# Optimization experiments

Hardware: AMD Instinct MI355X
Metric: run time of the kernel (lower is better)

## Reference

```python
import jax, jax.numpy as jnp
import numpy as np
from jax import lax

KERNEL = 2
STACKS = 2
LAYERS = 10
DILATIONS = [2 ** l for _ in range(STACKS) for l in range(LAYERS)]  # 20 blocks
RECEPTIVE_FIELD = sum((KERNEL - 1) * d for d in DILATIONS)  # 2046


def setup_inputs() -> dict:
    key = jax.random.key(0)
    ks = jax.random.split(key, 8)
    B, L, C, NC = 8, 4096, 256, 256
    NB = len(DILATIONS)
    SK = L - RECEPTIVE_FIELD  # 2050

    def rn(k, shape, scale):
        return jax.random.normal(k, shape, jnp.float32) * scale

    return {
        "input_x": jax.random.normal(ks[0], (B, L, 1), jnp.float32),
        "causal_w": rn(ks[1], (1, C), 1.0),                 # 1x1 causal conv, in=1
        "causal_b": jnp.zeros((C,), jnp.float32),
        "dil_w": rn(ks[2], (NB, KERNEL, C, C), (KERNEL * C) ** -0.5),  # WIO per block
        "dil_b": jnp.zeros((NB, C), jnp.float32),
        "res_w": rn(ks[3], (NB, C, C), C ** -0.5),
        "res_b": jnp.zeros((NB, C), jnp.float32),
        "skip_w": rn(ks[4], (NB, C, C), C ** -0.5),
        "skip_b": jnp.zeros((NB, C), jnp.float32),
        "cls_conv_w": rn(ks[5], (C, C), C ** -0.5),
        "cls_conv_b": jnp.zeros((C,), jnp.float32),
        "dense_w": rn(ks[6], (SK * C, NC), (SK * C) ** -0.5),
        "dense_b": jnp.zeros((NC,), jnp.float32),
    }


def _conv1x1(x, w, b):
    # x: [B, T, Cin], w: [Cin, Cout]
    return jnp.einsum("btc,co->bto", x, w) + b


def _dilated_causal_conv(x, w, b, d):
    # keras 'causal' pad followed by slicing off the first (k-1)*d frames
    # is exactly a VALID dilated conv. x: [B,T,Cin], w: [K,Cin,Cout]
    y = lax.conv_general_dilated(
        x, w, window_strides=(1,), padding="VALID", rhs_dilation=(d,),
        dimension_numbers=("NWC", "WIO", "NWC"))
    return y + b


def reference(input_x, causal_w, causal_b, dil_w, dil_b, res_w, res_b,
              skip_w, skip_b, cls_conv_w, cls_conv_b, dense_w, dense_b):
    # initial causal conv (kernel_size=1 -> plain 1x1 conv)
    x = _conv1x1(input_x, causal_w, causal_b)  # [B, L, C]
    skip_size = x.shape[1] - RECEPTIVE_FIELD

    skips = []
    for i, d in enumerate(DILATIONS):
        h = _dilated_causal_conv(x, dil_w[i], dil_b[i], d)  # [B, T-(k-1)d, C]
        g = jnp.tanh(h) * jax.nn.sigmoid(h)                  # gated activation
        res = _conv1x1(g, res_w[i], res_b[i])
        x = res + g                                          # residual (same length)
        s = _conv1x1(g, skip_w[i], skip_b[i])[:, -skip_size:]
        skips.append(s)

    # classifier head: mean over blocks, relu, shared 1x1 conv twice, dense+softmax
    s = jnp.mean(jnp.stack(skips, 0), axis=0)  # [B, skip_size, C]
    s = jax.nn.relu(s)
    s = _conv1x1(s, cls_conv_w, cls_conv_b)
    s = jax.nn.relu(s)
    s = _conv1x1(s, cls_conv_w, cls_conv_b)    # same conv applied twice (shared weights)
    f = s.reshape(s.shape[0], -1)              # flatten [B, skip_size*C]
    logits = f @ dense_w + dense_b
    return jax.nn.softmax(logits, axis=-1)
```

## Files before the change

### kernel.cpp

```cpp
#include <hip/hip_runtime.h>

typedef __attribute__((ext_vector_type(8))) short short8;
typedef __attribute__((ext_vector_type(4))) float f32x4;
typedef unsigned int uint32;
typedef unsigned short u16;

#define CCH   256
#define BATCH 8
#define LFULL 4096
#define SKL   2050
#define BM    128
#define BN    128
#define LDK   72

#define GSTRIDE ((size_t)BATCH * LFULL * CCH)
#define XSTR    ((size_t)LFULL * CCH)
#define SSTR    ((size_t)SKL * CCH)
#define PSTR    ((size_t)BATCH * SKL * CCH)

__device__ const int TOUT[20] = {4095,4093,4089,4081,4065,4033,3969,3841,3585,3073,
                                 3072,3070,3066,3058,3042,3010,2946,2818,2562,2050};

__device__ __forceinline__ u16 f2b(float f) {
  uint32 u = __float_as_uint(f);
  u += 0x7fff + ((u >> 16) & 1);
  return (u16)(u >> 16);
}
__device__ __forceinline__ float gatef(float h) {
  float hc = fmaxf(h, -30.0f);
  float q = __expf(-hc);
  return (1.0f - q) * __builtin_amdgcn_rcpf(fmaf(q, q, 1.0f));
}
__device__ __forceinline__ void glds16(const void* g, void* l) {
  __builtin_amdgcn_global_load_lds(
      (const __attribute__((address_space(1))) void*)g,
      (__attribute__((address_space(3))) void*)l, 16, 0, 0);
}

__global__ __launch_bounds__(256)
void compose_w(const float* __restrict__ res_w, const float* __restrict__ dil_w,
               u16* __restrict__ DWc) {
  __shared__ float As[32][256];
  int bx = blockIdx.x;
  int chunk = bx & 7, tap = (bx >> 3) & 1, bi = bx >> 4;
  int i = bi + 1;
  int co = threadIdx.x;
  int ci0 = chunk * 32;

  for (int idx = threadIdx.x; idx < 32 * 256; idx += 256) {
    int r = idx >> 8, m = idx & 255;
    float v = res_w[((size_t)(bi * 256 + ci0 + r)) * 256 + m];
    if (ci0 + r == m) v += 1.0f;
    As[r][m] = v;
  }
  __syncthreads();

  float acc[32];
  #pragma unroll
  for (int r = 0; r < 32; ++r) acc[r] = 0.0f;

  const float* Wb = dil_w + ((size_t)(i * 2 + tap) * 256) * 256 + co;
  for (int m4 = 0; m4 < 64; ++m4) {
    const float* wp = Wb + (size_t)m4 * 4 * 256;
    float w0 = wp[0], w1 = wp[256], w2 = wp[512], w3 = wp[768];
    #pragma unroll
    for (int r = 0; r < 32; ++r) {
      float4 a = *(const float4*)&As[r][m4 * 4];
      acc[r] = fmaf(a.x, w0, acc[r]);
      acc[r] = fmaf(a.y, w1, acc[r]);
      acc[r] = fmaf(a.z, w2, acc[r]);
      acc[r] = fmaf(a.w, w3, acc[r]);
    }
  }
  u16* op = DWc + ((size_t)(bi * 256 + co)) * 512 + tap * 256 + ci0;
  #pragma unroll
  for (int r = 0; r < 32; ++r) op[r] = f2b(acc[r]);
}

__global__ __launch_bounds__(256)
void compose_bias(const float* __restrict__ res_b, const float* __restrict__ dil_w,
                  const float* __restrict__ dil_b, float* __restrict__ Bc) {
  int bi = blockIdx.x, i = bi + 1, co = threadIdx.x;
  float acc = dil_b[(size_t)i * 256 + co];
  const float* W0 = dil_w + ((size_t)(i * 2 + 0) * 256) * 256;
  const float* W1 = dil_w + ((size_t)(i * 2 + 1) * 256) * 256;
  for (int m = 0; m < 256; ++m) {
    float rb = res_b[(size_t)bi * 256 + m];
    acc = fmaf(rb, W0[(size_t)m * 256 + co] + W1[(size_t)m * 256 + co], acc);
  }
  Bc[(size_t)bi * 256 + co] = acc;
}

__global__ __launch_bounds__(256)
void head0(const float* __restrict__ causal_w, const float* __restrict__ causal_b,
           const float* __restrict__ dil_w, const float* __restrict__ dil_b,
           float* __restrict__ U) {
  int co = threadIdx.x;
  float u0 = 0.f, u1 = 0.f, b0 = dil_b[co];
  for (int m = 0; m < 256; ++m) {
    float cwm = causal_w[m], cbm = causal_b[m];
    float w0 = dil_w[(size_t)m * 256 + co];
    float w1 = dil_w[(size_t)(256 + m) * 256 + co];
    u0 = fmaf(cwm, w0, u0);
    u1 = fmaf(cwm, w1, u1);
    b0 = fmaf(cbm, w0 + w1, b0);
  }
  U[co] = u0; U[256 + co] = u1; U[512 + co] = b0;
}

__global__ __launch_bounds__(256)
void g0_init(const float* __restrict__ in, const float* __restrict__ U,
             u16* __restrict__ G0) {
  int t = blockIdx.x, b = blockIdx.y, co = threadIdx.x;
  float x0 = in[(size_t)b * LFULL + t];
  float x1 = in[(size_t)b * LFULL + t + 1];
  float h = fmaf(x0, U[co], fmaf(x1, U[256 + co], U[512 + co]));
  G0[((size_t)b * LFULL + t) * CCH + co] = f2b(gatef(h));
}

__global__ __launch_bounds__(256)
void pack_skipT(const float* __restrict__ w, u16* __restrict__ o) {
  int e = blockIdx.x * 256 + threadIdx.x;
  int co = e & 255, ci = (e >> 8) & 255, i = e >> 16;
  o[(size_t)co * 5120 + i * 256 + ci] = f2b(w[e]);
}
__global__ __launch_bounds__(256)
void pack_cls(const float* __restrict__ w, u16* __restrict__ o) {
  int e = blockIdx.x * 256 + threadIdx.x;
  int co = e & 255, ci = e >> 8;
  o[(size_t)co * 256 + ci] = f2b(w[e]);
}
__global__ __launch_bounds__(256)
void sbsum_k(const float* __restrict__ sb, float* __restrict__ o) {
  int n = threadIdx.x;
  float s = 0.f;
  for (int i = 0; i < 20; ++i) s += sb[(size_t)i * 256 + n];
  o[n] = s;
}

__global__ __launch_bounds__(256)
void gatem(const u16* __restrict__ Ain, int d,
           const u16* __restrict__ Wt, const float* __restrict__ bias,
           u16* __restrict__ Out1, int Tout) {
  __shared__ u16 As[BM * 64];
  __shared__ u16 Bs[BN * 64];

  const int tid = threadIdx.x;
  const int bb  = blockIdx.z;
  const int t0  = blockIdx.x * BM;
  const int n0  = blockIdx.y * BN;
  const int lane = tid & 63, wv = tid >> 6;
  const int wm = wv >> 1, wn = wv & 1;
  const int fr = lane & 15, fq = lane >> 4;
  const int rl = lane >> 3;
  const int subx = ((lane & 7) ^ rl) * 8;

  const u16* Ab = Ain + (size_t)bb * XSTR;

  f32x4 acc[4][4];
  #pragma unroll
  for (int fn = 0; fn < 4; ++fn) {
    float bv = bias[n0 + wn * 64 + fn * 16 + fr];
    #pragma unroll
    for (int fm = 0; fm < 4; ++fm) acc[fm][fn] = (f32x4){bv, bv, bv, bv};
  }

  for (int kt = 0; kt < 8; ++kt) {
    const int tap = kt >> 2, ks0 = (kt & 3) * 64;
    const int rowb = wv * 32;
    #pragma unroll
    for (int q = 0; q < 4; ++q) {
      int t = t0 + rowb + q * 8 + rl;
      if (t > Tout - 1) t = Tout - 1;
      glds16(Ab + (size_t)(t + tap * d) * CCH + ks0 + subx,
             As + (rowb + q * 8) * 64);
      glds16(Wt + (size_t)(n0 + rowb + q * 8 + rl) * 512 + kt * 64 + subx,
             Bs + (rowb + q * 8) * 64);
    }
    __syncthreads();

    #pragma unroll
    for (int ks = 0; ks < 2; ++ks) {
      short8 af[4], bfr[4];
      #pragma unroll
      for (int fm = 0; fm < 4; ++fm) {
        int row = wm * 64 + fm * 16 + fr;
        af[fm] = *(const short8*)&As[row * 64 + ((ks * 4 + fq) ^ (row & 7)) * 8];
      }
      #pragma unroll
      for (int fn = 0; fn < 4; ++fn) {
        int row = wn * 64 + fn * 16 + fr;
        bfr[fn] = *(const short8*)&Bs[row * 64 + ((ks * 4 + fq) ^ (row & 7)) * 8];
      }
      #pragma unroll
      for (int fm = 0; fm < 4; ++fm)
        #pragma unroll
        for (int fn = 0; fn < 4; ++fn)
          acc[fm][fn] = __builtin_amdgcn_mfma_f32_16x16x32_bf16(
              af[fm], bfr[fn], acc[fm][fn], 0, 0, 0);
    }
    __syncthreads();
  }

  u16* Ob = Out1 + (size_t)bb * XSTR;
  #pragma unroll
  for (int fm = 0; fm < 4; ++fm) {
    int rbase = t0 + wm * 64 + fm * 16 + fq * 4;
    #pragma unroll
    for (int r = 0; r < 4; ++r) {
      int t = rbase + r;
      if (t >= Tout) continue;
      #pragma unroll
      for (int fn = 0; fn < 4; ++fn) {
        int c = n0 + wn * 64 + fn * 16 + fr;
        Ob[(size_t)t * CCH + c] = f2b(gatef(acc[fm][fn][r]));
      }
    }
  }
}

__global__ __launch_bounds__(256)
void skipm(const u16* __restrict__ Gh, const u16* __restrict__ SWT,
           float* __restrict__ P) {
  __shared__ u16 As[BM * 64];
  __shared__ u16 Bs[BN * 64];

  const int tid = threadIdx.x;
  const int zz = blockIdx.z;
  const int b = zz >> 2, j = zz & 3;
  const int t0 = blockIdx.x * BM;
  const int n0 = blockIdx.y * BN;
  const int lane = tid & 63, wv = tid >> 6;
  const int wm = wv >> 1, wn = wv & 1;
  const int fr = lane & 15, fq = lane >> 4;
  const int rl = lane >> 3;
  const int subx = ((lane & 7) ^ rl) * 8;

  f32x4 acc[4][4];
  #pragma unroll
  for (int fm = 0; fm < 4; ++fm)
    #pragma unroll
    for (int fn = 0; fn < 4; ++fn) acc[fm][fn] = (f32x4){0.f, 0.f, 0.f, 0.f};

  for (int kt = 0; kt < 20; ++kt) {
    const int i = j * 5 + (kt >> 2);
    const int toff = TOUT[i] - SKL;
    const int ks0 = (kt & 3) * 64;
    const u16* Gi = Gh + (size_t)i * GSTRIDE + (size_t)b * XSTR;
    const int rowb = wv * 32;
    #pragma unroll
    for (int q = 0; q < 4; ++q) {
      int t = t0 + rowb + q * 8 + rl;
      if (t > SKL - 1) t = SKL - 1;
      glds16(Gi + (size_t)(toff + t) * CCH + ks0 + subx,
             As + (rowb + q * 8) * 64);
      glds16(SWT + (size_t)(n0 + rowb + q * 8 + rl) * 5120 + i * 256 + ks0 + subx,
             Bs + (rowb + q * 8) * 64);
    }
    __syncthreads();

    #pragma unroll
    for (int ks = 0; ks < 2; ++ks) {
      short8 af[4], bfr[4];
      #pragma unroll
      for (int fm = 0; fm < 4; ++fm) {
        int row = wm * 64 + fm * 16 + fr;
        af[fm] = *(const short8*)&As[row * 64 + ((ks * 4 + fq) ^ (row & 7)) * 8];
      }
      #pragma unroll
      for (int fn = 0; fn < 4; ++fn) {
        int row = wn * 64 + fn * 16 + fr;
        bfr[fn] = *(const short8*)&Bs[row * 64 + ((ks * 4 + fq) ^ (row & 7)) * 8];
      }
      #pragma unroll
      for (int fm = 0; fm < 4; ++fm)
        #pragma unroll
        for (int fn = 0; fn < 4; ++fn)
          acc[fm][fn] = __builtin_amdgcn_mfma_f32_16x16x32_bf16(
              af[fm], bfr[fn], acc[fm][fn], 0, 0, 0);
    }
    __syncthreads();
  }

  float* Pj = P + (size_t)(j * BATCH + b) * SSTR;
  #pragma unroll
  for (int fm = 0; fm < 4; ++fm) {
    int rbase = t0 + wm * 64 + fm * 16 + fq * 4;
    #pragma unroll
    for (int r = 0; r < 4; ++r) {
      int t = rbase + r;
      if (t >= SKL) continue;
      #pragma unroll
      for (int fn = 0; fn < 4; ++fn) {
        int c = n0 + wn * 64 + fn * 16 + fr;
        Pj[(size_t)t * CCH + c] = acc[fm][fn][r];
      }
    }
  }
}

enum { MODE_CLS1 = 1, MODE_CLS2 = 2 };

template <int MODE>
__global__ __launch_bounds__(256)
void convm(const void* __restrict__ Ainv, long a_bstride,
           const u16* __restrict__ Wt, const float* __restrict__ bias,
           const float* __restrict__ extra,
           void* __restrict__ Out1, long out_bstride, int Tout) {
  __shared__ u16 As[BM * LDK];
  __shared__ u16 Bs[BN * LDK];

  const int tid = threadIdx.x;
  const int bb  = blockIdx.z;
  const int t0  = blockIdx.x * BM;
  const int n0  = blockIdx.y * BN;
  const int lane = tid & 63, wv = tid >> 6;
  const int wm = wv >> 1, wn = wv & 1;
  const int fr = lane & 15, fq = lane >> 4;

  f32x4 acc[4][4];
  #pragma unroll
  for (int fn = 0; fn < 4; ++fn) {
    float bv = bias[n0 + wn * 64 + fn * 16 + fr];
    #pragma unroll
    for (int fm = 0; fm < 4; ++fm) acc[fm][fn] = (f32x4){bv, bv, bv, bv};
  }

  for (int kt = 0; kt < 4; ++kt) {
    for (int idx = tid; idx < 1024; idx += 256) {
      int r = idx >> 3, c8 = idx & 7;
      int t = t0 + r; if (t > Tout - 1) t = Tout - 1;
      uint4 v;
      if constexpr (MODE == MODE_CLS1) {
        const float* p0 = (const float*)Ainv + (size_t)bb * a_bstride +
                          (size_t)t * CCH + kt * 64 + c8 * 8;
        float4 s0 = *(const float4*)p0;
        float4 s1 = *(const float4*)(p0 + 4);
        #pragma unroll
        for (int jj = 1; jj < 4; ++jj) {
          const float* pj = p0 + (size_t)jj * PSTR;
          float4 a0 = *(const float4*)pj;
          float4 a1 = *(const float4*)(pj + 4);
          s0.x += a0.x; s0.y += a0.y; s0.z += a0.z; s0.w += a0.w;
          s1.x += a1.x; s1.y += a1.y; s1.z += a1.z; s1.w += a1.w;
        }
        float4 e0 = *(const float4*)&extra[kt * 64 + c8 * 8];
        float4 e1 = *(const float4*)&extra[kt * 64 + c8 * 8 + 4];
        u16 tmp[8];
        tmp[0] = f2b(fmaxf((s0.x + e0.x) * 0.05f, 0.f));
        tmp[1] = f2b(fmaxf((s0.y + e0.y) * 0.05f, 0.f));
        tmp[2] = f2b(fmaxf((s0.z + e0.z) * 0.05f, 0.f));
        tmp[3] = f2b(fmaxf((s0.w + e0.w) * 0.05f, 0.f));
        tmp[4] = f2b(fmaxf((s1.x + e1.x) * 0.05f, 0.f));
        tmp[5] = f2b(fmaxf((s1.y + e1.y) * 0.05f, 0.f));
        tmp[6] = f2b(fmaxf((s1.z + e1.z) * 0.05f, 0.f));
        tmp[7] = f2b(fmaxf((s1.w + e1.w) * 0.05f, 0.f));
        v = *(uint4*)tmp;
      } else {
        const u16* sp = (const u16*)Ainv + (size_t)bb * a_bstride +
                        (size_t)t * CCH + kt * 64 + c8 * 8;
        uint4 raw = *(const uint4*)sp;
        u16 tmp[8];
        *(uint4*)tmp = raw;
        #pragma unroll
        for (int jj = 0; jj < 8; ++jj) tmp[jj] = (tmp[jj] & 0x8000) ? (u16)0 : tmp[jj];
        v = *(uint4*)tmp;
      }
      *(uint4*)&As[r * LDK + c8 * 8] = v;
    }
    for (int idx = tid; idx < 1024; idx += 256) {
      int r = idx >> 3, c8 = idx & 7;
      const u16* sp = Wt + (size_t)(n0 + r) * 256 + kt * 64 + c8 * 8;
      *(uint4*)&Bs[r * LDK + c8 * 8] = *(const uint4*)sp;
    }
    __syncthreads();

    #pragma unroll
    for (int ks = 0; ks < 2; ++ks) {
      short8 af[4], bfr[4];
      #pragma unroll
      for (int fm = 0; fm < 4; ++fm)
        af[fm] = *(const short8*)&As[(wm * 64 + fm * 16 + fr) * LDK + ks * 32 + fq * 8];
      #pragma unroll
      for (int fn = 0; fn < 4; ++fn)
        bfr[fn] = *(const short8*)&Bs[(wn * 64 + fn * 16 + fr) * LDK + ks * 32 + fq * 8];
      #pragma unroll
      for (int fm = 0; fm < 4; ++fm)
        #pragma unroll
        for (int fn = 0; fn < 4; ++fn)
          acc[fm][fn] = __builtin_amdgcn_mfma_f32_16x16x32_bf16(
              af[fm], bfr[fn], acc[fm][fn], 0, 0, 0);
    }
    __syncthreads();
  }

  #pragma unroll
  for (int fm = 0; fm < 4; ++fm) {
    int rbase = t0 + wm * 64 + fm * 16 + fq * 4;
    #pragma unroll
    for (int r = 0; r < 4; ++r) {
      int t = rbase + r;
      if (t >= Tout) continue;
      #pragma unroll
      for (int fn = 0; fn < 4; ++fn) {
        int c = n0 + wn * 64 + fn * 16 + fr;
        float a = acc[fm][fn][r];
        size_t oix = (size_t)bb * out_bstride + (size_t)t * CCH + c;
        if constexpr (MODE == MODE_CLS1) {
          ((u16*)Out1)[oix] = f2b(a);
        } else {
          ((float*)Out1)[oix] = a;
        }
      }
    }
  }
}

__global__ __launch_bounds__(256)
void dense_partial(const float* __restrict__ f, const float* __restrict__ W,
                   float* __restrict__ part) {
  int tstep = blockIdx.x;
  int n = threadIdx.x;
  __shared__ float fs[BATCH][CCH];
  for (int idx = threadIdx.x; idx < BATCH * CCH; idx += 256) {
    int b = idx >> 8, c = idx & 255;
    fs[b][c] = f[((size_t)b * SKL + tstep) * CCH + c];
  }
  __syncthreads();
  float acc[BATCH] = {0.f, 0.f, 0.f, 0.f, 0.f, 0.f, 0.f, 0.f};
  const float* Wr = W + (size_t)tstep * CCH * CCH;
  for (int ci = 0; ci < CCH; ++ci) {
    float w = Wr[(size_t)ci * CCH + n];
    #pragma unroll
    for (int b = 0; b < BATCH; ++b) acc[b] = fmaf(fs[b][ci], w, acc[b]);
  }
  #pragma unroll
  for (int b = 0; b < BATCH; ++b)
    part[((size_t)tstep * BATCH + b) * CCH + n] = acc[b];
}

__global__ __launch_bounds__(256)
void reduce_part(const float* __restrict__ part, float* __restrict__ part2) {
  int chunk = blockIdx.x, b = blockIdx.y, n = threadIdx.x;
  int c0 = chunk * 33;
  int c1 = c0 + 33; if (c1 > SKL) c1 = SKL;
  float s = 0.f;
  for (int c = c0; c < c1; ++c) s += part[((size_t)c * BATCH + b) * CCH + n];
  part2[((size_t)b * 64 + chunk) * CCH + n] = s;
}

__global__ __launch_bounds__(256)
void softmax_k(const float* __restrict__ part2, const float* __restrict__ db,
               float* __restrict__ out) {
  int b = blockIdx.x, n = threadIdx.x;
  float s = db[n];
  for (int ch = 0; ch < 64; ++ch) s += part2[((size_t)b * 64 + ch) * CCH + n];

  __shared__ float r4[4];
  __shared__ float mglob, sglob;
  int wid = n >> 6, lane = n & 63;

  float m = s;
  #pragma unroll
  for (int off = 1; off < 64; off <<= 1) m = fmaxf(m, __shfl_xor(m, off));
  if (lane == 0) r4[wid] = m;
  __syncthreads();
  if (n == 0) mglob = fmaxf(fmaxf(r4[0], r4[1]), fmaxf(r4[2], r4[3]));
  __syncthreads();

  float e = expf(s - mglob);
  float se = e;
  #pragma unroll
  for (int off = 1; off < 64; off <<= 1) se += __shfl_xor(se, off);
  if (lane == 0) r4[wid] = se;
  __syncthreads();
  if (n == 0) sglob = r4[0] + r4[1] + r4[2] + r4[3];
  __syncthreads();

  out[(size_t)b * CCH + n] = e / sglob;
}

extern "C" void kernel_launch(void* const* d_in, const int* in_sizes, int n_in,
                              void* d_out, int out_size, void* d_ws, size_t ws_size,
                              hipStream_t stream) {
  const float* input_x  = (const float*)d_in[0];
  const float* causal_w = (const float*)d_in[1];
  const float* causal_b = (const float*)d_in[2];
  const float* dil_w    = (const float*)d_in[3];
  const float* dil_b    = (const float*)d_in[4];
  const float* res_w    = (const float*)d_in[5];
  const float* res_b    = (const float*)d_in[6];
  const float* skip_w   = (const float*)d_in[7];
  const float* skip_b   = (const float*)d_in[8];
  const float* cls_w    = (const float*)d_in[9];
  const float* cls_b    = (const float*)d_in[10];
  const float* dense_w  = (const float*)d_in[11];
  const float* dense_b  = (const float*)d_in[12];
  float* out = (float*)d_out;

  char* p = (char*)d_ws;
  u16*   Gh    = (u16*)p;   p += GSTRIDE * 20 * 2;
  float* P     = (float*)p; p += PSTR * 4 * 4;
  u16*   S1    = (u16*)p;   p += (size_t)BATCH * SKL * CCH * 2;
  float* S2    = (float*)p; p += (size_t)BATCH * SKL * CCH * 4;
  float* PART  = (float*)p; p += (size_t)SKL * BATCH * CCH * 4;
  float* PART2 = (float*)p; p += (size_t)BATCH * 64 * CCH * 4;
  u16*   DWc   = (u16*)p;   p += (size_t)19 * 256 * 512 * 2;
  float* Bc    = (float*)p; p += (size_t)19 * 256 * 4;
  u16*   SWT   = (u16*)p;   p += (size_t)256 * 5120 * 2;
  u16*   CW    = (u16*)p;   p += (size_t)256 * 256 * 2;
  float* U     = (float*)p; p += (size_t)768 * 4;
  float* SBS   = (float*)p; p += (size_t)256 * 4;

  static const int dil[20] = {1, 2, 4, 8, 16, 32, 64, 128, 256, 512,
                              1, 2, 4, 8, 16, 32, 64, 128, 256, 512};
  static const int tout_h[20] = {4095,4093,4089,4081,4065,4033,3969,3841,3585,3073,
                                 3072,3070,3066,3058,3042,3010,2946,2818,2562,2050};
  dim3 blk(256);

  compose_w   <<<dim3(19 * 2 * 8), blk, 0, stream>>>(res_w, dil_w, DWc);
  compose_bias<<<dim3(19), blk, 0, stream>>>(res_b, dil_w, dil_b, Bc);
  head0       <<<dim3(1), blk, 0, stream>>>(causal_w, causal_b, dil_w, dil_b, U);
  pack_skipT  <<<dim3(20 * 256), blk, 0, stream>>>(skip_w, SWT);
  pack_cls    <<<dim3(256), blk, 0, stream>>>(cls_w, CW);
  sbsum_k     <<<dim3(1), blk, 0, stream>>>(skip_b, SBS);

  g0_init<<<dim3(4095, BATCH), blk, 0, stream>>>(input_x, U, Gh);

  for (int i = 1; i < 20; ++i) {
    int Tout = tout_h[i];
    int ntile = (Tout + BM - 1) / BM;
    gatem<<<dim3(ntile, 2, BATCH), blk, 0, stream>>>(
        Gh + (size_t)(i - 1) * GSTRIDE, dil[i],
        DWc + (size_t)(i - 1) * 256 * 512, Bc + (size_t)(i - 1) * 256,
        Gh + (size_t)i * GSTRIDE, Tout);
  }

  int stile = (SKL + BM - 1) / BM;
  skipm<<<dim3(stile, 2, BATCH * 4), blk, 0, stream>>>(Gh, SWT, P);

  convm<MODE_CLS1><<<dim3(stile, 2, BATCH), blk, 0, stream>>>(
      P, (long)SSTR, CW, cls_b, SBS, S1, (long)SSTR, SKL);
  convm<MODE_CLS2><<<dim3(stile, 2, BATCH), blk, 0, stream>>>(
      S1, (long)SSTR, CW, cls_b, nullptr, S2, (long)SSTR, SKL);

  dense_partial<<<dim3(SKL), blk, 0, stream>>>(S2, dense_w, PART);
  reduce_part<<<dim3(64, BATCH), blk, 0, stream>>>(PART, PART2);
  softmax_k<<<dim3(BATCH), blk, 0, stream>>>(PART2, dense_b, out);
}
```

Measured before the change: 718.5 us.

## Fuse per-layer skip GEMM into gate kernel launches with in-place accumulation

```diff
diff --git a/kernel.cpp b/kernel.cpp
--- a/kernel.cpp
+++ b/kernel.cpp
@@ -16,10 +16,6 @@
 #define GSTRIDE ((size_t)BATCH * LFULL * CCH)
 #define XSTR    ((size_t)LFULL * CCH)
 #define SSTR    ((size_t)SKL * CCH)
-#define PSTR    ((size_t)BATCH * SKL * CCH)
-
-__device__ const int TOUT[20] = {4095,4093,4089,4081,4065,4033,3969,3841,3585,3073,
-                                 3072,3070,3066,3058,3042,3010,2946,2818,2562,2050};
 
 __device__ __forceinline__ u16 f2b(float f) {
   uint32 u = __float_as_uint(f);
@@ -139,15 +135,15 @@
 }
 
 __global__ __launch_bounds__(256)
-void gatem(const u16* __restrict__ Ain, int d,
-           const u16* __restrict__ Wt, const float* __restrict__ bias,
-           u16* __restrict__ Out1, int Tout) {
+void gatesk(const u16* __restrict__ Ain, int d, int Tout, int ntile,
+            const u16* __restrict__ Wt, const float* __restrict__ bias,
+            u16* __restrict__ Gout,
+            const u16* __restrict__ SWTi, int toff, float* __restrict__ P) {
   __shared__ u16 As[BM * 64];
   __shared__ u16 Bs[BN * 64];
 
   const int tid = threadIdx.x;
   const int bb  = blockIdx.z;
-  const int t0  = blockIdx.x * BM;
   const int n0  = blockIdx.y * BN;
   const int lane = tid & 63, wv = tid >> 6;
   const int wm = wv >> 1, wn = wv & 1;
@@ -155,27 +151,45 @@
   const int rl = lane >> 3;
   const int subx = ((lane & 7) ^ rl) * 8;
 
+  const bool isgate = (int)blockIdx.x < ntile;
+  const int t0 = (isgate ? blockIdx.x : blockIdx.x - ntile) * BM;
   const u16* Ab = Ain + (size_t)bb * XSTR;
 
   f32x4 acc[4][4];
-  #pragma unroll
-  for (int fn = 0; fn < 4; ++fn) {
-    float bv = bias[n0 + wn * 64 + fn * 16 + fr];
-    #pragma unroll
-    for (int fm = 0; fm < 4; ++fm) acc[fm][fn] = (f32x4){bv, bv, bv, bv};
-  }
-
-  for (int kt = 0; kt < 8; ++kt) {
-    const int tap = kt >> 2, ks0 = (kt & 3) * 64;
+  if (isgate) {
+    #pragma unroll
+    for (int fn = 0; fn < 4; ++fn) {
+      float4 bv = *(const float4*)&bias[n0 + wn * 64 + fn * 16 + fq * 4];
+      #pragma unroll
+      for (int fm = 0; fm < 4; ++fm) acc[fm][fn] = (f32x4){bv.x, bv.y, bv.z, bv.w};
+    }
+  } else {
+    #pragma unroll
+    for (int fm = 0; fm < 4; ++fm)
+      #pragma unroll
+      for (int fn = 0; fn < 4; ++fn) acc[fm][fn] = (f32x4){0.f, 0.f, 0.f, 0.f};
+  }
+
+  const int KT = isgate ? 8 : 4;
+  for (int kt = 0; kt < KT; ++kt) {
+    const int ks0 = (kt & 3) * 64;
     const int rowb = wv * 32;
     #pragma unroll
     for (int q = 0; q < 4; ++q) {
-      int t = t0 + rowb + q * 8 + rl;
-      if (t > Tout - 1) t = Tout - 1;
-      glds16(Ab + (size_t)(t + tap * d) * CCH + ks0 + subx,
-             As + (rowb + q * 8) * 64);
-      glds16(Wt + (size_t)(n0 + rowb + q * 8 + rl) * 512 + kt * 64 + subx,
-             Bs + (rowb + q * 8) * 64);
+      int rr = rowb + q * 8 + rl;
+      int t = t0 + rr;
+      const u16 *asrc, *bsrc;
+      if (isgate) {
+        if (t > Tout - 1) t = Tout - 1;
+        asrc = Ab + (size_t)(t + (kt >> 2) * d) * CCH + ks0 + subx;
+        bsrc = Wt + (size_t)(n0 + rr) * 512 + kt * 64 + subx;
+      } else {
+        if (t > SKL - 1) t = SKL - 1;
+        asrc = Ab + (size_t)(toff + t) * CCH + ks0 + subx;
+        bsrc = SWTi + (size_t)(n0 + rr) * 5120 + kt * 64 + subx;
+      }
+      glds16(asrc, As + (rowb + q * 8) * 64);
+      glds16(bsrc, Bs + (rowb + q * 8) * 64);
     }
     __syncthreads();
 
@@ -197,103 +211,41 @@
         #pragma unroll
         for (int fn = 0; fn < 4; ++fn)
           acc[fm][fn] = __builtin_amdgcn_mfma_f32_16x16x32_bf16(
-              af[fm], bfr[fn], acc[fm][fn], 0, 0, 0);
+              bfr[fn], af[fm], acc[fm][fn], 0, 0, 0);
     }
     __syncthreads();
   }
 
-  u16* Ob = Out1 + (size_t)bb * XSTR;
-  #pragma unroll
-  for (int fm = 0; fm < 4; ++fm) {
-    int rbase = t0 + wm * 64 + fm * 16 + fq * 4;
-    #pragma unroll
-    for (int r = 0; r < 4; ++r) {
-      int t = rbase + r;
+  if (isgate) {
+    u16* Ob = Gout + (size_t)bb * XSTR;
+    #pragma unroll
+    for (int fm = 0; fm < 4; ++fm) {
+      int t = t0 + wm * 64 + fm * 16 + fr;
       if (t >= Tout) continue;
       #pragma unroll
       for (int fn = 0; fn < 4; ++fn) {
-        int c = n0 + wn * 64 + fn * 16 + fr;
-        Ob[(size_t)t * CCH + c] = f2b(gatef(acc[fm][fn][r]));
-      }
-    }
-  }
-}
-
-__global__ __launch_bounds__(256)
-void skipm(const u16* __restrict__ Gh, const u16* __restrict__ SWT,
-           float* __restrict__ P) {
-  __shared__ u16 As[BM * 64];
-  __shared__ u16 Bs[BN * 64];
-
-  const int tid = threadIdx.x;
-  const int zz = blockIdx.z;
-  const int b = zz >> 2, j = zz & 3;
-  const int t0 = blockIdx.x * BM;
-  const int n0 = blockIdx.y * BN;
-  const int lane = tid & 63, wv = tid >> 6;
-  const int wm = wv >> 1, wn = wv & 1;
-  const int fr = lane & 15, fq = lane >> 4;
-  const int rl = lane >> 3;
-  const int subx = ((lane & 7) ^ rl) * 8;
-
-  f32x4 acc[4][4];
-  #pragma unroll
-  for (int fm = 0; fm < 4; ++fm)
-    #pragma unroll
-    for (int fn = 0; fn < 4; ++fn) acc[fm][fn] = (f32x4){0.f, 0.f, 0.f, 0.f};
-
-  for (int kt = 0; kt < 20; ++kt) {
-    const int i = j * 5 + (kt >> 2);
-    const int toff = TOUT[i] - SKL;
-    const int ks0 = (kt & 3) * 64;
-    const u16* Gi = Gh + (size_t)i * GSTRIDE + (size_t)b * XSTR;
-    const int rowb = wv * 32;
-    #pragma unroll
-    for (int q = 0; q < 4; ++q) {
-      int t = t0 + rowb + q * 8 + rl;
-      if (t > SKL - 1) t = SKL - 1;
-      glds16(Gi + (size_t)(toff + t) * CCH + ks0 + subx,
-             As + (rowb + q * 8) * 64);
-      glds16(SWT + (size_t)(n0 + rowb + q * 8 + rl) * 5120 + i * 256 + ks0 + subx,
-             Bs + (rowb + q * 8) * 64);
-    }
-    __syncthreads();
-
-    #pragma unroll
-    for (int ks = 0; ks < 2; ++ks) {
-      short8 af[4], bfr[4];
-      #pragma unroll
-      for (int fm = 0; fm < 4; ++fm) {
-        int row = wm * 64 + fm * 16 + fr;
-        af[fm] = *(const short8*)&As[row * 64 + ((ks * 4 + fq) ^ (row & 7)) * 8];
-      }
+        int c0 = n0 + wn * 64 + fn * 16 + fq * 4;
+        f32x4 a = acc[fm][fn];
+        uint32 p0 = (uint32)f2b(gatef(a[0])) | ((uint32)f2b(gatef(a[1])) << 16);
+        uint32 p1 = (uint32)f2b(gatef(a[2])) | ((uint32)f2b(gatef(a[3])) << 16);
+        uint2 pk; pk.x = p0; pk.y = p1;
+        *(uint2*)(Ob + (size_t)t * CCH + c0) = pk;
+      }
+    }
+  } else {
+    float* Pb = P + (size_t)bb * SSTR;
+    #pragma unroll
+    for (int fm = 0; fm < 4; ++fm) {
+      int t = t0 + wm * 64 + fm * 16 + fr;
+      if (t >= SKL) continue;
       #pragma unroll
       for (int fn = 0; fn < 4; ++fn) {
-        int row = wn * 64 + fn * 16 + fr;
-        bfr[fn] = *(const short8*)&Bs[row * 64 + ((ks * 4 + fq) ^ (row & 7)) * 8];
-      }
-      #pragma unroll
-      for (int fm = 0; fm < 4; ++fm)
-        #pragma unroll
-        for (int fn = 0; fn < 4; ++fn)
-          acc[fm][fn] = __builtin_amdgcn_mfma_f32_16x16x32_bf16(
-              af[fm], bfr[fn], acc[fm][fn], 0, 0, 0);
-    }
-    __syncthreads();
-  }
-
-  float* Pj = P + (size_t)(j * BATCH + b) * SSTR;
-  #pragma unroll
-  for (int fm = 0; fm < 4; ++fm) {
-    int rbase = t0 + wm * 64 + fm * 16 + fq * 4;
-    #pragma unroll
-    for (int r = 0; r < 4; ++r) {
-      int t = rbase + r;
-      if (t >= SKL) continue;
-      #pragma unroll
-      for (int fn = 0; fn < 4; ++fn) {
-        int c = n0 + wn * 64 + fn * 16 + fr;
-        Pj[(size_t)t * CCH + c] = acc[fm][fn][r];
+        int c0 = n0 + wn * 64 + fn * 16 + fq * 4;
+        float4* pp = (float4*)(Pb + (size_t)t * CCH + c0);
+        float4 old = *pp;
+        f32x4 a = acc[fm][fn];
+        old.x += a[0]; old.y += a[1]; old.z += a[2]; old.w += a[3];
+        *pp = old;
       }
     }
   }
@@ -336,14 +288,6 @@
                           (size_t)t * CCH + kt * 64 + c8 * 8;
         float4 s0 = *(const float4*)p0;
         float4 s1 = *(const float4*)(p0 + 4);
-        #pragma unroll
-        for (int jj = 1; jj < 4; ++jj) {
-          const float* pj = p0 + (size_t)jj * PSTR;
-          float4 a0 = *(const float4*)pj;
-          float4 a1 = *(const float4*)(pj + 4);
-          s0.x += a0.x; s0.y += a0.y; s0.z += a0.z; s0.w += a0.w;
-          s1.x += a1.x; s1.y += a1.y; s1.z += a1.z; s1.w += a1.w;
-        }
         float4 e0 = *(const float4*)&extra[kt * 64 + c8 * 8];
         float4 e1 = *(const float4*)&extra[kt * 64 + c8 * 8 + 4];
         u16 tmp[8];
@@ -500,7 +444,7 @@
 
   char* p = (char*)d_ws;
   u16*   Gh    = (u16*)p;   p += GSTRIDE * 20 * 2;
-  float* P     = (float*)p; p += PSTR * 4 * 4;
+  float* P     = (float*)p; p += (size_t)BATCH * SKL * CCH * 4;
   u16*   S1    = (u16*)p;   p += (size_t)BATCH * SKL * CCH * 2;
   float* S2    = (float*)p; p += (size_t)BATCH * SKL * CCH * 4;
   float* PART  = (float*)p; p += (size_t)SKL * BATCH * CCH * 4;
@@ -517,6 +461,7 @@
   static const int tout_h[20] = {4095,4093,4089,4081,4065,4033,3969,3841,3585,3073,
                                  3072,3070,3066,3058,3042,3010,2946,2818,2562,2050};
   dim3 blk(256);
+  const int stile = (SKL + BM - 1) / BM;
 
   compose_w   <<<dim3(19 * 2 * 8), blk, 0, stream>>>(res_w, dil_w, DWc);
   compose_bias<<<dim3(19), blk, 0, stream>>>(res_b, dil_w, dil_b, Bc);
@@ -525,19 +470,22 @@
   pack_cls    <<<dim3(256), blk, 0, stream>>>(cls_w, CW);
   sbsum_k     <<<dim3(1), blk, 0, stream>>>(skip_b, SBS);
 
+  hipMemsetAsync(P, 0, (size_t)BATCH * SKL * CCH * 4, stream);
   g0_init<<<dim3(4095, BATCH), blk, 0, stream>>>(input_x, U, Gh);
 
   for (int i = 1; i < 20; ++i) {
     int Tout = tout_h[i];
     int ntile = (Tout + BM - 1) / BM;
-    gatem<<<dim3(ntile, 2, BATCH), blk, 0, stream>>>(
-        Gh + (size_t)(i - 1) * GSTRIDE, dil[i],
+    gatesk<<<dim3(ntile + stile, 2, BATCH), blk, 0, stream>>>(
+        Gh + (size_t)(i - 1) * GSTRIDE, dil[i], Tout, ntile,
         DWc + (size_t)(i - 1) * 256 * 512, Bc + (size_t)(i - 1) * 256,
-        Gh + (size_t)i * GSTRIDE, Tout);
-  }
-
-  int stile = (SKL + BM - 1) / BM;
-  skipm<<<dim3(stile, 2, BATCH * 4), blk, 0, stream>>>(Gh, SWT, P);
+        Gh + (size_t)i * GSTRIDE,
+        SWT + (size_t)(i - 1) * 256, tout_h[i - 1] - SKL, P);
+  }
+  gatesk<<<dim3(stile, 2, BATCH), blk, 0, stream>>>(
+      Gh + (size_t)19 * GSTRIDE, 0, SKL, 0,
+      DWc, Bc, Gh + (size_t)19 * GSTRIDE,
+      SWT + (size_t)19 * 256, tout_h[19] - SKL, P);
 
   convm<MODE_CLS1><<<dim3(stile, 2, BATCH), blk, 0, stream>>>(
       P, (long)SSTR, CW, cls_b, SBS, S1, (long)SSTR, SKL);
```

New measurement: 759.3 us. 5.7% more time.

## Double-buffer LDS loads, XCD-swizzle grid, and vectorize epilogue in gate/skip GEMMs

Applied to the files above, without the earlier changes.

```diff
diff --git a/kernel.cpp b/kernel.cpp
--- a/kernel.cpp
+++ b/kernel.cpp
@@ -35,6 +35,12 @@
   __builtin_amdgcn_global_load_lds(
       (const __attribute__((address_space(1))) void*)g,
       (__attribute__((address_space(3))) void*)l, 16, 0, 0);
+}
+__device__ __forceinline__ int xcd_swz(int orig, int nwg) {
+  int xcd = orig & 7, idx = orig >> 3;
+  int q = nwg >> 3, r = nwg & 7;
+  int base = (xcd < r) ? xcd * (q + 1) : r * (q + 1) + (xcd - r) * q;
+  return base + idx;
 }
 
 __global__ __launch_bounds__(256)
@@ -139,45 +145,64 @@
 }
 
 __global__ __launch_bounds__(256)
-void gatem(const u16* __restrict__ Ain, int d,
+void gatem(const u16* __restrict__ Ain, int d, int Tout, int ntile,
            const u16* __restrict__ Wt, const float* __restrict__ bias,
-           u16* __restrict__ Out1, int Tout) {
-  __shared__ u16 As[BM * 64];
-  __shared__ u16 Bs[BN * 64];
+           u16* __restrict__ Gout) {
+  __shared__ u16 As[2][BM * 64];
+  __shared__ u16 Bs[2][BN * 64];
 
   const int tid = threadIdx.x;
-  const int bb  = blockIdx.z;
-  const int t0  = blockIdx.x * BM;
-  const int n0  = blockIdx.y * BN;
+  const int nwg = ntile * 16;
+  const int wgid = xcd_swz(blockIdx.x, nwg);
+  const int tx = wgid % ntile;
+  const int rem = wgid / ntile;
+  const int ny = rem & 1;
+  const int bb = rem >> 1;
+
+  const int t0 = tx * BM;
+  const int n0 = ny * BN;
   const int lane = tid & 63, wv = tid >> 6;
   const int wm = wv >> 1, wn = wv & 1;
   const int fr = lane & 15, fq = lane >> 4;
   const int rl = lane >> 3;
   const int subx = ((lane & 7) ^ rl) * 8;
+  const int rowb = wv * 32;
 
   const u16* Ab = Ain + (size_t)bb * XSTR;
 
   f32x4 acc[4][4];
   #pragma unroll
   for (int fn = 0; fn < 4; ++fn) {
-    float bv = bias[n0 + wn * 64 + fn * 16 + fr];
-    #pragma unroll
-    for (int fm = 0; fm < 4; ++fm) acc[fm][fn] = (f32x4){bv, bv, bv, bv};
-  }
-
-  for (int kt = 0; kt < 8; ++kt) {
+    float4 bv = *(const float4*)&bias[n0 + wn * 64 + fn * 16 + fq * 4];
+    #pragma unroll
+    for (int fm = 0; fm < 4; ++fm) acc[fm][fn] = (f32x4){bv.x, bv.y, bv.z, bv.w};
+  }
+
+  auto STAGE = [&](int kt, int sel) {
     const int tap = kt >> 2, ks0 = (kt & 3) * 64;
-    const int rowb = wv * 32;
-    #pragma unroll
-    for (int q = 0; q < 4; ++q) {
-      int t = t0 + rowb + q * 8 + rl;
+    #pragma unroll
+    for (int qq = 0; qq < 4; ++qq) {
+      int rr = rowb + qq * 8 + rl;
+      int t = t0 + rr;
       if (t > Tout - 1) t = Tout - 1;
       glds16(Ab + (size_t)(t + tap * d) * CCH + ks0 + subx,
-             As + (rowb + q * 8) * 64);
-      glds16(Wt + (size_t)(n0 + rowb + q * 8 + rl) * 512 + kt * 64 + subx,
-             Bs + (rowb + q * 8) * 64);
-    }
-    __syncthreads();
+             &As[sel][(rowb + qq * 8) * 64]);
+      glds16(Wt + (size_t)(n0 + rr) * 512 + kt * 64 + subx,
+             &Bs[sel][(rowb + qq * 8) * 64]);
+    }
+  };
+
+  STAGE(0, 0);
+  for (int kt = 0; kt < 8; ++kt) {
+    const int cur = kt & 1;
+    if (kt < 7) {
+      STAGE(kt + 1, cur ^ 1);
+      asm volatile("s_waitcnt vmcnt(8)" ::: "memory");
+    } else {
+      asm volatile("s_waitcnt vmcnt(0)" ::: "memory");
+    }
+    __builtin_amdgcn_s_barrier();
+    __builtin_amdgcn_sched_barrier(0);
 
     #pragma unroll
     for (int ks = 0; ks < 2; ++ks) {
@@ -185,36 +210,36 @@
       #pragma unroll
       for (int fm = 0; fm < 4; ++fm) {
         int row = wm * 64 + fm * 16 + fr;
-        af[fm] = *(const short8*)&As[row * 64 + ((ks * 4 + fq) ^ (row & 7)) * 8];
+        af[fm] = *(const short8*)&As[cur][row * 64 + ((ks * 4 + fq) ^ (row & 7)) * 8];
       }
       #pragma unroll
       for (int fn = 0; fn < 4; ++fn) {
         int row = wn * 64 + fn * 16 + fr;
-        bfr[fn] = *(const short8*)&Bs[row * 64 + ((ks * 4 + fq) ^ (row & 7)) * 8];
+        bfr[fn] = *(const short8*)&Bs[cur][row * 64 + ((ks * 4 + fq) ^ (row & 7)) * 8];
       }
       #pragma unroll
       for (int fm = 0; fm < 4; ++fm)
         #pragma unroll
         for (int fn = 0; fn < 4; ++fn)
           acc[fm][fn] = __builtin_amdgcn_mfma_f32_16x16x32_bf16(
-              af[fm], bfr[fn], acc[fm][fn], 0, 0, 0);
-    }
-    __syncthreads();
-  }
-
-  u16* Ob = Out1 + (size_t)bb * XSTR;
+              bfr[fn], af[fm], acc[fm][fn], 0, 0, 0);
+    }
+    __builtin_amdgcn_s_barrier();
+  }
+
+  u16* Ob = Gout + (size_t)bb * XSTR;
   #pragma unroll
   for (int fm = 0; fm < 4; ++fm) {
-    int rbase = t0 + wm * 64 + fm * 16 + fq * 4;
-    #pragma unroll
-    for (int r = 0; r < 4; ++r) {
-      int t = rbase + r;
-      if (t >= Tout) continue;
-      #pragma unroll
-      for (int fn = 0; fn < 4; ++fn) {
-        int c = n0 + wn * 64 + fn * 16 + fr;
-        Ob[(size_t)t * CCH + c] = f2b(gatef(acc[fm][fn][r]));
-      }
+    int t = t0 + wm * 64 + fm * 16 + fr;
+    if (t >= Tout) continue;
+    #pragma unroll
+    for (int fn = 0; fn < 4; ++fn) {
+      int c0 = n0 + wn * 64 + fn * 16 + fq * 4;
+      f32x4 a = acc[fm][fn];
+      uint32 p0 = (uint32)f2b(gatef(a[0])) | ((uint32)f2b(gatef(a[1])) << 16);
+      uint32 p1 = (uint32)f2b(gatef(a[2])) | ((uint32)f2b(gatef(a[3])) << 16);
+      uint2 pk; pk.x = p0; pk.y = p1;
+      *(uint2*)(Ob + (size_t)t * CCH + c0) = pk;
     }
   }
 }
@@ -222,19 +247,26 @@
 __global__ __launch_bounds__(256)
 void skipm(const u16* __restrict__ Gh, const u16* __restrict__ SWT,
            float* __restrict__ P) {
-  __shared__ u16 As[BM * 64];
-  __shared__ u16 Bs[BN * 64];
+  __shared__ u16 As[2][BM * 64];
+  __shared__ u16 Bs[2][BN * 64];
 
   const int tid = threadIdx.x;
-  const int zz = blockIdx.z;
+  const int nwg = 17 * 2 * 32;
+  const int wgid = xcd_swz(blockIdx.x, nwg);
+  const int tx = wgid % 17;
+  const int rem = wgid / 17;
+  const int ny = rem & 1;
+  const int zz = rem >> 1;
   const int b = zz >> 2, j = zz & 3;
-  const int t0 = blockIdx.x * BM;
-  const int n0 = blockIdx.y * BN;
+
+  const int t0 = tx * BM;
+  const int n0 = ny * BN;
   const int lane = tid & 63, wv = tid >> 6;
   const int wm = wv >> 1, wn = wv & 1;
   const int fr = lane & 15, fq = lane >> 4;
   const int rl = lane >> 3;
   const int subx = ((lane & 7) ^ rl) * 8;
+  const int rowb = wv * 32;
 
   f32x4 acc[4][4];
   #pragma unroll
@@ -242,22 +274,34 @@
     #pragma unroll
     for (int fn = 0; fn < 4; ++fn) acc[fm][fn] = (f32x4){0.f, 0.f, 0.f, 0.f};
 
-  for (int kt = 0; kt < 20; ++kt) {
+  auto STAGE = [&](int kt, int sel) {
     const int i = j * 5 + (kt >> 2);
     const int toff = TOUT[i] - SKL;
     const int ks0 = (kt & 3) * 64;
     const u16* Gi = Gh + (size_t)i * GSTRIDE + (size_t)b * XSTR;
-    const int rowb = wv * 32;
-    #pragma unroll
-    for (int q = 0; q < 4; ++q) {
-      int t = t0 + rowb + q * 8 + rl;
+    #pragma unroll
+    for (int qq = 0; qq < 4; ++qq) {
+      int rr = rowb + qq * 8 + rl;
+      int t = t0 + rr;
       if (t > SKL - 1) t = SKL - 1;
       glds16(Gi + (size_t)(toff + t) * CCH + ks0 + subx,
-             As + (rowb + q * 8) * 64);
-      glds16(SWT + (size_t)(n0 + rowb + q * 8 + rl) * 5120 + i * 256 + ks0 + subx,
-             Bs + (rowb + q * 8) * 64);
-    }
-    __syncthreads();
+             &As[sel][(rowb + qq * 8) * 64]);
+      glds16(SWT + (size_t)(n0 + rr) * 5120 + i * 256 + ks0 + subx,
+             &Bs[sel][(rowb + qq * 8) * 64]);
+    }
+  };
+
+  STAGE(0, 0);
+  for (int kt = 0; kt < 20; ++kt) {
+    const int cur = kt & 1;
+    if (kt < 19) {
+      STAGE(kt + 1, cur ^ 1);
+      asm volatile("s_waitcnt vmcnt(8)" ::: "memory");
+    } else {
+      asm volatile("s_waitcnt vmcnt(0)" ::: "memory");
+    }
+    __builtin_amdgcn_s_barrier();
+    __builtin_amdgcn_sched_barrier(0);
 
     #pragma unroll
     for (int ks = 0; ks < 2; ++ks) {
@@ -265,36 +309,34 @@
       #pragma unroll
       for (int fm = 0; fm < 4; ++fm) {
         int row = wm * 64 + fm * 16 + fr;
-        af[fm] = *(const short8*)&As[row * 64 + ((ks * 4 + fq) ^ (row & 7)) * 8];
+        af[fm] = *(const short8*)&As[cur][row * 64 + ((ks * 4 + fq) ^ (row & 7)) * 8];
       }
       #pragma unroll
       for (int fn = 0; fn < 4; ++fn) {
         int row = wn * 64 + fn * 16 + fr;
-        bfr[fn] = *(const short8*)&Bs[row * 64 + ((ks * 4 + fq) ^ (row & 7)) * 8];
+        bfr[fn] = *(const short8*)&Bs[cur][row * 64 + ((ks * 4 + fq) ^ (row & 7)) * 8];
       }
       #pragma unroll
       for (int fm = 0; fm < 4; ++fm)
         #pragma unroll
         for (int fn = 0; fn < 4; ++fn)
           acc[fm][fn] = __builtin_amdgcn_mfma_f32_16x16x32_bf16(
-              af[fm], bfr[fn], acc[fm][fn], 0, 0, 0);
-    }
-    __syncthreads();
-  }
-
-  float* Pj = P + (size_t)(j * BATCH + b) * SSTR;
+              bfr[fn], af[fm], acc[fm][fn], 0, 0, 0);
+    }
+    __builtin_amdgcn_s_barrier();
+  }
+
+  float* Pj = P + (size_t)j * PSTR + (size_t)b * SSTR;
   #pragma unroll
   for (int fm = 0; fm < 4; ++fm) {
-    int rbase = t0 + wm * 64 + fm * 16 + fq * 4;
-    #pragma unroll
-    for (int r = 0; r < 4; ++r) {
-      int t = rbase + r;
-      if (t >= SKL) continue;
-      #pragma unroll
-      for (int fn = 0; fn < 4; ++fn) {
-        int c = n0 + wn * 64 + fn * 16 + fr;
-        Pj[(size_t)t * CCH + c] = acc[fm][fn][r];
-      }
+    int t = t0 + wm * 64 + fm * 16 + fr;
+    if (t >= SKL) continue;
+    #pragma unroll
+    for (int fn = 0; fn < 4; ++fn) {
+      int c0 = n0 + wn * 64 + fn * 16 + fq * 4;
+      f32x4 a = acc[fm][fn];
+      float4 o = {a[0], a[1], a[2], a[3]};
+      *(float4*)(Pj + (size_t)t * CCH + c0) = o;
     }
   }
 }
@@ -517,6 +559,7 @@
   static const int tout_h[20] = {4095,4093,4089,4081,4065,4033,3969,3841,3585,3073,
                                  3072,3070,3066,3058,3042,3010,2946,2818,2562,2050};
   dim3 blk(256);
+  const int stile = (SKL + BM - 1) / BM;
 
   compose_w   <<<dim3(19 * 2 * 8), blk, 0, stream>>>(res_w, dil_w, DWc);
   compose_bias<<<dim3(19), blk, 0, stream>>>(res_b, dil_w, dil_b, Bc);
@@ -530,14 +573,13 @@
   for (int i = 1; i < 20; ++i) {
     int Tout = tout_h[i];
     int ntile = (Tout + BM - 1) / BM;
-    gatem<<<dim3(ntile, 2, BATCH), blk, 0, stream>>>(
-        Gh + (size_t)(i - 1) * GSTRIDE, dil[i],
+    gatem<<<dim3(ntile * 16), blk, 0, stream>>>(
+        Gh + (size_t)(i - 1) * GSTRIDE, dil[i], Tout, ntile,
         DWc + (size_t)(i - 1) * 256 * 512, Bc + (size_t)(i - 1) * 256,
-        Gh + (size_t)i * GSTRIDE, Tout);
-  }
-
-  int stile = (SKL + BM - 1) / BM;
-  skipm<<<dim3(stile, 2, BATCH * 4), blk, 0, stream>>>(Gh, SWT, P);
+        Gh + (size_t)i * GSTRIDE);
+  }
+
+  skipm<<<dim3(17 * 2 * 32), blk, 0, stream>>>(Gh, SWT, P);
 
   convm<MODE_CLS1><<<dim3(stile, 2, BATCH), blk, 0, stream>>>(
       P, (long)SSTR, CW, cls_b, SBS, S1, (long)SSTR, SKL);
```

After: 703.8 us. -2.0%, faster.
